# Performance work log

Hardware: AMD Instinct MI355X
Metric: run time of the kernel (lower is better)

The kernel has to match this reference:

```python
import jax, jax.numpy as jnp
import numpy as np

LN_EPS = 1e-5
NEG_INF = -1e38

def _layer_norm(x, g, b):
    mu = x.mean(-1, keepdims=True)
    var = ((x - mu) ** 2).mean(-1, keepdims=True)
    return (x - mu) * jax.lax.rsqrt(var + LN_EPS) * g + b

def _wkv(w, u, k, v):
    # w,u: [C]; k,v: [B,T,C]. Numerically-stable RWKV WKV scan over T.
    B, T, C = k.shape
    kt = jnp.swapaxes(k, 0, 1)  # [T,B,C]
    vt = jnp.swapaxes(v, 0, 1)
    aa0 = jnp.zeros((B, C), k.dtype)
    bb0 = jnp.zeros((B, C), k.dtype)
    pp0 = jnp.full((B, C), NEG_INF, k.dtype)

    def step(carry, inp):
        aa, bb, pp = carry
        kk, vv = inp
        p = jnp.maximum(pp, u + kk)
        e1 = jnp.exp(pp - p)
        e2 = jnp.exp(u + kk - p)
        y = (e1 * aa + e2 * vv) / (e1 + e2)
        p2 = jnp.maximum(pp + w, w + kk)
        e1u = jnp.exp(pp + w - p2)
        e2u = jnp.exp(w + kk - p2)
        aa2 = e1u * aa + e2u * vv
        bb2 = e1u + e2u
        pp2 = p2 + jnp.log(bb2)
        return (aa2, bb2, pp2), y

    _, ys = jax.lax.scan(step, (aa0, bb0, pp0), (kt, vt))
    return jnp.swapaxes(ys, 0, 1)  # [B,T,C]

def _shift(h):
    # x_prev: zero-pad one step at the front (state=None path)
    return jnp.pad(h[:, :-1, :], ((0, 0), (1, 0), (0, 0)))

def setup_inputs() -> dict:
    key = jax.random.key(0)
    B, T, C = 8, 2048, 1024
    ks = jax.random.split(key, 12)
    s = 0.02
    return {
        "x": jax.random.normal(ks[0], (B, T, C), jnp.float32),
        "time_decay": jax.random.normal(ks[1], (C,), jnp.float32) * 0.01,
        "time_first": jax.random.normal(ks[2], (C,), jnp.float32) * 0.01,
        "w_tk": jax.random.normal(ks[3], (C, C), jnp.float32) * s,
        "w_tv": jax.random.normal(ks[4], (C, C), jnp.float32) * s,
        "w_tr": jax.random.normal(ks[5], (C, C), jnp.float32) * s,
        "w_ck": jax.random.normal(ks[6], (C, 4 * C), jnp.float32) * s,
        "w_cv": jax.random.normal(ks[7], (4 * C, C), jnp.float32) * s,
        "w_cr": jax.random.normal(ks[8], (C, C), jnp.float32) * s,
        "ln1_g": jnp.ones((C,), jnp.float32),
        "ln1_b": jnp.zeros((C,), jnp.float32),
        "ln2_g": jnp.ones((C,), jnp.float32),
        "ln2_b": jnp.zeros((C,), jnp.float32),
        "mix_k": jnp.ones((1, 1, C), jnp.float32),
        "mix_v": jnp.ones((1, 1, C), jnp.float32),
        "mix_r": jnp.ones((1, 1, C), jnp.float32),
        "cmix_k": jnp.ones((1, 1, C), jnp.float32),
        "cmix_r": jnp.ones((1, 1, C), jnp.float32),
    }

def reference(x, time_decay, time_first, w_tk, w_tv, w_tr, w_ck, w_cv, w_cr,
              ln1_g, ln1_b, ln2_g, ln2_b, mix_k, mix_v, mix_r, cmix_k, cmix_r):
    # --- time mixing (residual branch 1); dropout is identity at eval ---
    h = _layer_norm(x, ln1_g, ln1_b)
    hp = _shift(h)
    xk = h * mix_k + hp * (1.0 - mix_k)
    xv = h * mix_v + hp * (1.0 - mix_v)
    xr = h * mix_r + hp * (1.0 - mix_r)
    k = xk @ w_tk
    v = xv @ w_tv
    r = jax.nn.sigmoid(xr @ w_tr)
    y = _wkv(time_decay, time_first, k, v)
    x = x + r * y
    # --- channel mixing (residual branch 2) ---
    h2 = _layer_norm(x, ln2_g, ln2_b)
    hp2 = _shift(h2)
    ck = h2 * cmix_k + hp2 * (1.0 - cmix_k)
    cr = h2 * cmix_r + hp2 * (1.0 - cmix_r)
    kk = jnp.square(jax.nn.relu(ck @ w_ck))  # [B,T,4C]
    x = x + jax.nn.sigmoid(cr @ w_cr) * (kk @ w_cv)
    return x
```

## Files before the change

kernel.cpp:

```cpp
#include <hip/hip_runtime.h>
#include <hip/hip_bf16.h>
#include <stdint.h>

#define LN_EPS 1e-5f

typedef __attribute__((ext_vector_type(8))) __bf16 bf16x8;
typedef __attribute__((ext_vector_type(8))) short short8;
typedef __attribute__((ext_vector_type(4))) float floatx4;

__device__ __forceinline__ ushort f2bf(float f) {
    __hip_bfloat16 h = __float2bfloat16(f);
    return *reinterpret_cast<ushort*>(&h);
}
__device__ __forceinline__ float bf2f(ushort u) {
    return __builtin_bit_cast(float, ((unsigned int)u) << 16);
}

__device__ __forceinline__ void gload16(const void* g, void* l) {
#if __has_builtin(__builtin_amdgcn_global_load_lds)
    __builtin_amdgcn_global_load_lds(
        (const __attribute__((address_space(1))) unsigned int*)g,
        (__attribute__((address_space(3))) unsigned int*)l, 16, 0, 0);
#else
    *(int4*)l = *(const int4*)g;
#endif
}

#define SBAR __builtin_amdgcn_s_barrier()
#define SCHED0 __builtin_amdgcn_sched_barrier(0)
#define WAIT_LGKM0 asm volatile("s_waitcnt lgkmcnt(0)" ::: "memory")
#define WAIT_VM4 asm volatile("s_waitcnt vmcnt(4)" ::: "memory")
#define WAIT_VM0 asm volatile("s_waitcnt vmcnt(0)" ::: "memory")

#define STAGE_A(h, t)                                                        \
    do {                                                                     \
        ushort* _d = &lds[((((t) & 1) * 2 + 0) * 2 + (h)) * 8192];           \
        const long _o = (long)(h) * 128 * lda + (long)(t) * 64;              \
        gload16(aS0 + _o, _d + tid * 8);                                     \
        gload16(aS1 + _o, _d + (tid + 512) * 8);                             \
    } while (0)
#define STAGE_B(h, t)                                                        \
    do {                                                                     \
        ushort* _d = &lds[((((t) & 1) * 2 + 1) * 2 + (h)) * 8192];           \
        const long _o = (long)(h) * 128 * ldb + (long)(t) * 64;              \
        gload16(bS0 + _o, _d + tid * 8);                                     \
        gload16(bS1 + _o, _d + (tid + 512) * 8);                             \
    } while (0)
#define GEMM_LDA(MB)                                                         \
    _Pragma("unroll") for (int mi = 0; mi < 4; ++mi)                         \
    _Pragma("unroll") for (int ks = 0; ks < 2; ++ks)                         \
        a[mi][ks] = __builtin_bit_cast(                                      \
            bf16x8, *(const short8*)&ldsA[((MB) + mi) * 1024 + ks * 512 + aoff]);
#define GEMM_LDB(NB)                                                         \
    _Pragma("unroll") for (int ni = 0; ni < 2; ++ni)                         \
    _Pragma("unroll") for (int ks = 0; ks < 2; ++ks)                         \
        b[(NB) + ni][ks] = __builtin_bit_cast(                               \
            bf16x8, *(const short8*)&ldsB[((NB) + ni) * 1024 + ks * 512 + boff]);
#define GEMM_MFMA(MB, NB)                                                    \
    __builtin_amdgcn_s_setprio(1);                                           \
    _Pragma("unroll") for (int mi = 0; mi < 4; ++mi)                         \
    _Pragma("unroll") for (int ni = 0; ni < 2; ++ni)                         \
    _Pragma("unroll") for (int ks = 0; ks < 2; ++ks)                         \
        acc[(MB) + mi][(NB) + ni] = __builtin_amdgcn_mfma_f32_16x16x32_bf16( \
            a[mi][ks], b[(NB) + ni][ks], acc[(MB) + mi][(NB) + ni], 0, 0, 0);\
    __builtin_amdgcn_s_setprio(0);

template <int EPI>
__global__ __launch_bounds__(512, 2) void gemm256(
    const ushort* __restrict__ A, const ushort* __restrict__ Bt,
    int K, int lda, int ldb, int ldc,
    float* __restrict__ outF, ushort* __restrict__ outB,
    const float* __restrict__ add0, const ushort* __restrict__ mul0) {
    extern __shared__ ushort lds[];

    const int tid  = threadIdx.x;
    const int lane = tid & 63;
    const int quad = lane >> 4;
    const int l16  = lane & 15;
    const int wv   = tid >> 6;
    const int wmi  = wv >> 2;
    const int wni  = wv & 3;
    const long m0 = (long)blockIdx.y * 256;
    const long n0 = (long)blockIdx.x * 256;

    floatx4 acc[8][4];
#pragma unroll
    for (int i = 0; i < 8; ++i)
#pragma unroll
        for (int j = 0; j < 4; ++j) acc[i][j] = (floatx4)0.f;

    const int j1 = tid + 512;
    const int r0 = ((tid >> 7) << 4) + (tid & 15);
    const int c0 = (tid >> 4) & 7;
    const int col0 = (c0 & 3) * 8 + (c0 >> 2) * 32;
    const int r1 = ((j1 >> 7) << 4) + (j1 & 15);
    const int c1 = (j1 >> 4) & 7;
    const int col1 = (c1 & 3) * 8 + (c1 >> 2) * 32;
    const ushort* aS0 = A + (m0 + r0) * (long)lda + col0;
    const ushort* aS1 = A + (m0 + r1) * (long)lda + col1;
    const ushort* bS0 = Bt + (n0 + r0) * (long)ldb + col0;
    const ushort* bS1 = Bt + (n0 + r1) * (long)ldb + col1;

    const int aoff = quad * 128 + l16 * 8;
    const int boff = (wni & 1) * 4096 + quad * 128 + l16 * 8;

    const int NT = K >> 6;

    STAGE_A(0, 0); STAGE_A(1, 0);
    STAGE_B(0, 0); STAGE_B(1, 0);
    if (NT > 1) { STAGE_B(0, 1); STAGE_B(1, 1); WAIT_VM4; }
    else        { WAIT_VM0; }
    SBAR;

    bf16x8 a[4][2], b[4][2];
    for (int kt = 0; kt < NT; ++kt) {
        const int d = kt & 1;
        const ushort* ldsA = &lds[((d * 2 + 0) * 2 + wmi) * 8192];
        const ushort* ldsB = &lds[((d * 2 + 1) * 2 + (wni >> 1)) * 8192];

        GEMM_LDA(0)
        GEMM_LDB(0)
        if (kt + 1 < NT) STAGE_A(0, kt + 1);
        SBAR; WAIT_LGKM0; SCHED0;
        GEMM_MFMA(0, 0)
        SCHED0; SBAR;

        GEMM_LDB(2)
        if (kt + 1 < NT) STAGE_A(1, kt + 1);
        SBAR; WAIT_LGKM0; SCHED0;
        GEMM_MFMA(0, 2)
        SCHED0; SBAR;

        GEMM_LDA(4)
        if (kt + 2 < NT) STAGE_B(0, kt + 2);
        SBAR; WAIT_LGKM0; SCHED0;
        GEMM_MFMA(4, 2)
        SCHED0; SBAR;

        if (kt + 2 < NT) STAGE_B(1, kt + 2);
        if (kt < NT - 2) { WAIT_VM4; } else { WAIT_VM0; }
        SBAR; SCHED0;
        GEMM_MFMA(4, 0)
        SCHED0; SBAR;
    }

#pragma unroll
    for (int mi = 0; mi < 8; ++mi) {
#pragma unroll
        for (int ni = 0; ni < 4; ++ni) {
            const long n = n0 + wni * 64 + ni * 16 + l16;
#pragma unroll
            for (int r = 0; r < 4; ++r) {
                const long m = m0 + wmi * 128 + mi * 16 + quad * 4 + r;
                const long idx = m * (long)ldc + n;
                float v = acc[mi][ni][r];
                if constexpr (EPI == 0) {
                    outB[idx] = f2bf(v);
                } else if constexpr (EPI == 1) {
                    outB[idx] = f2bf(1.f / (1.f + __expf(-v)));
                } else if constexpr (EPI == 2) {
                    float t = fmaxf(v, 0.f);
                    outB[idx] = f2bf(t * t);
                } else if constexpr (EPI == 3) {
                    outF[idx] = add0[idx] + bf2f(mul0[idx]) * v;
                }
            }
        }
    }
}

__global__ __launch_bounds__(256) void ln_mix3(
    const float* __restrict__ x, const float* __restrict__ g,
    const float* __restrict__ be,
    const float* __restrict__ mx0, const float* __restrict__ mx1,
    const float* __restrict__ mx2,
    ushort* __restrict__ o0, ushort* __restrict__ o1, ushort* __restrict__ o2,
    int T, int C) {
    const long row = blockIdx.x;
    const int t = (int)(row % T);
    const int tid = threadIdx.x;
    const int i0 = tid * 4;

    floatx4 xc = *(const floatx4*)&x[row * C + i0];
    floatx4 xp = (floatx4)0.f;
    if (t > 0) xp = *(const floatx4*)&x[(row - 1) * C + i0];

    float sc = xc.x + xc.y + xc.z + xc.w;
    float qc = xc.x * xc.x + xc.y * xc.y + xc.z * xc.z + xc.w * xc.w;
    float sp = xp.x + xp.y + xp.z + xp.w;
    float qp = xp.x * xp.x + xp.y * xp.y + xp.z * xp.z + xp.w * xp.w;

#pragma unroll
    for (int off = 32; off; off >>= 1) {
        sc += __shfl_xor(sc, off);
        qc += __shfl_xor(qc, off);
        sp += __shfl_xor(sp, off);
        qp += __shfl_xor(qp, off);
    }
    __shared__ float part[4][4];
    const int wv = tid >> 6;
    if ((tid & 63) == 0) {
        part[wv][0] = sc; part[wv][1] = qc; part[wv][2] = sp; part[wv][3] = qp;
    }
    __syncthreads();
    sc = part[0][0] + part[1][0] + part[2][0] + part[3][0];
    qc = part[0][1] + part[1][1] + part[2][1] + part[3][1];
    sp = part[0][2] + part[1][2] + part[2][2] + part[3][2];
    qp = part[0][3] + part[1][3] + part[2][3] + part[3][3];

    const float invC = 1.f / (float)C;
    float muc = sc * invC;
    float rsc = rsqrtf(qc * invC - muc * muc + LN_EPS);
    float mup = sp * invC;
    float rsp = rsqrtf(qp * invC - mup * mup + LN_EPS);

    floatx4 gv = *(const floatx4*)&g[i0];
    floatx4 bv = *(const floatx4*)&be[i0];
    floatx4 hc = (xc - muc) * rsc * gv + bv;
    floatx4 hp = (floatx4)0.f;
    if (t > 0) hp = (xp - mup) * rsp * gv + bv;

    {
        floatx4 mk = *(const floatx4*)&mx0[i0];
        floatx4 v = hc * mk + hp * (1.f - mk);
        ushort4 pk;
        pk.x = f2bf(v.x); pk.y = f2bf(v.y); pk.z = f2bf(v.z); pk.w = f2bf(v.w);
        *(ushort4*)&o0[row * C + i0] = pk;
    }
    {
        floatx4 mk = *(const floatx4*)&mx1[i0];
        floatx4 v = hc * mk + hp * (1.f - mk);
        ushort4 pk;
        pk.x = f2bf(v.x); pk.y = f2bf(v.y); pk.z = f2bf(v.z); pk.w = f2bf(v.w);
        *(ushort4*)&o1[row * C + i0] = pk;
    }
    {
        floatx4 mk = *(const floatx4*)&mx2[i0];
        floatx4 v = hc * mk + hp * (1.f - mk);
        ushort4 pk;
        pk.x = f2bf(v.x); pk.y = f2bf(v.y); pk.z = f2bf(v.z); pk.w = f2bf(v.w);
        *(ushort4*)&o2[row * C + i0] = pk;
    }
}

__global__ __launch_bounds__(256) void ln_mix_add(
    const float* __restrict__ x, const ushort* __restrict__ ry,
    const float* __restrict__ g, const float* __restrict__ be,
    const float* __restrict__ mx0, const float* __restrict__ mx1,
    float* __restrict__ outx,
    ushort* __restrict__ o0, ushort* __restrict__ o1, int T, int C) {
    const long row = blockIdx.x;
    const int t = (int)(row % T);
    const int tid = threadIdx.x;
    const int i0 = tid * 4;

    floatx4 xc = *(const floatx4*)&x[row * C + i0];
    ushort4 rc = *(const ushort4*)&ry[row * C + i0];
    xc.x += bf2f(rc.x); xc.y += bf2f(rc.y); xc.z += bf2f(rc.z); xc.w += bf2f(rc.w);
    *(floatx4*)&outx[row * C + i0] = xc;

    floatx4 xp = (floatx4)0.f;
    if (t > 0) {
        xp = *(const floatx4*)&x[(row - 1) * C + i0];
        ushort4 rp = *(const ushort4*)&ry[(row - 1) * C + i0];
        xp.x += bf2f(rp.x); xp.y += bf2f(rp.y); xp.z += bf2f(rp.z); xp.w += bf2f(rp.w);
    }

    float sc = xc.x + xc.y + xc.z + xc.w;
    float qc = xc.x * xc.x + xc.y * xc.y + xc.z * xc.z + xc.w * xc.w;
    float sp = xp.x + xp.y + xp.z + xp.w;
    float qp = xp.x * xp.x + xp.y * xp.y + xp.z * xp.z + xp.w * xp.w;

#pragma unroll
    for (int off = 32; off; off >>= 1) {
        sc += __shfl_xor(sc, off);
        qc += __shfl_xor(qc, off);
        sp += __shfl_xor(sp, off);
        qp += __shfl_xor(qp, off);
    }
    __shared__ float part[4][4];
    const int wv = tid >> 6;
    if ((tid & 63) == 0) {
        part[wv][0] = sc; part[wv][1] = qc; part[wv][2] = sp; part[wv][3] = qp;
    }
    __syncthreads();
    sc = part[0][0] + part[1][0] + part[2][0] + part[3][0];
    qc = part[0][1] + part[1][1] + part[2][1] + part[3][1];
    sp = part[0][2] + part[1][2] + part[2][2] + part[3][2];
    qp = part[0][3] + part[1][3] + part[2][3] + part[3][3];

    const float invC = 1.f / (float)C;
    float muc = sc * invC;
    float rsc = rsqrtf(qc * invC - muc * muc + LN_EPS);
    float mup = sp * invC;
    float rsp = rsqrtf(qp * invC - mup * mup + LN_EPS);

    floatx4 gv = *(const floatx4*)&g[i0];
    floatx4 bv = *(const floatx4*)&be[i0];
    floatx4 hc = (xc - muc) * rsc * gv + bv;
    floatx4 hp = (floatx4)0.f;
    if (t > 0) hp = (xp - mup) * rsp * gv + bv;

    {
        floatx4 mk = *(const floatx4*)&mx0[i0];
        floatx4 v = hc * mk + hp * (1.f - mk);
        ushort4 pk;
        pk.x = f2bf(v.x); pk.y = f2bf(v.y); pk.z = f2bf(v.z); pk.w = f2bf(v.w);
        *(ushort4*)&o0[row * C + i0] = pk;
    }
    {
        floatx4 mk = *(const floatx4*)&mx1[i0];
        floatx4 v = hc * mk + hp * (1.f - mk);
        ushort4 pk;
        pk.x = f2bf(v.x); pk.y = f2bf(v.y); pk.z = f2bf(v.z); pk.w = f2bf(v.w);
        *(ushort4*)&o1[row * C + i0] = pk;
    }
}


__global__ __launch_bounds__(256) void wkv_pp_local(
    const float* __restrict__ w, const ushort* __restrict__ k,
    float* __restrict__ pp_loc, int C, int L) {
    const int g = blockIdx.x * 256 + threadIdx.x;
    const int c = g % C;
    const long seg = g / C;
    const float L2E = 1.4426950408889634f;
    const float w2 = w[c] * L2E;
    const ushort* kp = k + seg * L * C + c;
    float pp = -1e38f;
    for (int j = 0; j < L; ++j) {
        float kk = bf2f(kp[(long)j * C]) * L2E;
        float ppw = pp + w2;
        float wk = w2 + kk;
        float p2 = fmaxf(ppw, wk);
        pp = p2 + log2f(exp2f(ppw - p2) + exp2f(wk - p2));
    }
    pp_loc[g] = pp;
}

__global__ __launch_bounds__(256) void wkv_pp_compose(
    const float* __restrict__ w, const float* __restrict__ pp_loc,
    float* __restrict__ pp_in, int C, int SEG, int L) {
    const int g = blockIdx.x * 256 + threadIdx.x;
    const int c = g % C;
    const long b = g / C;
    const float wL = w[c] * 1.4426950408889634f * (float)L;
    float pp = -1e38f;
    for (int s = 0; s < SEG; ++s) {
        const long idx = (b * SEG + s) * C + c;
        pp_in[idx] = pp;
        float lhs = pp + wL;
        float rhs = pp_loc[idx];
        float m = fmaxf(lhs, rhs);
        pp = m + log2f(exp2f(lhs - m) + exp2f(rhs - m));
    }
}

__global__ __launch_bounds__(256) void wkv_ab_local(
    const float* __restrict__ w, const ushort* __restrict__ k,
    const ushort* __restrict__ v, const float* __restrict__ pp_in,
    float* __restrict__ alpha, float* __restrict__ beta, int C, int L) {
    const int g = blockIdx.x * 256 + threadIdx.x;
    const int c = g % C;
    const long seg = g / C;
    const float L2E = 1.4426950408889634f;
    const float w2 = w[c] * L2E;
    const ushort* kp = k + seg * L * C + c;
    const ushort* vp = v + seg * L * C + c;
    float pp = pp_in[g];
    float al = 1.f, be = 0.f;
    for (int j = 0; j < L; ++j) {
        float kk = bf2f(kp[(long)j * C]) * L2E;
        float vv = bf2f(vp[(long)j * C]);
        float ppw = pp + w2;
        float wk = w2 + kk;
        float p2 = fmaxf(ppw, wk);
        float e1u = exp2f(ppw - p2);
        float e2u = exp2f(wk - p2);
        al *= e1u;
        be = e1u * be + e2u * vv;
        pp = p2 + log2f(e1u + e2u);
    }
    alpha[g] = al;
    beta[g] = be;
}

__global__ __launch_bounds__(256) void wkv_aa_compose(
    const float* __restrict__ alpha, const float* __restrict__ beta,
    float* __restrict__ aa_in, int C, int SEG) {
    const int g = blockIdx.x * 256 + threadIdx.x;
    const int c = g % C;
    const long b = g / C;
    float aa = 0.f;
    for (int s = 0; s < SEG; ++s) {
        const long idx = (b * SEG + s) * C + c;
        aa_in[idx] = aa;
        aa = alpha[idx] * aa + beta[idx];
    }
    (void)c;
}

__global__ __launch_bounds__(256) void wkv_emit(
    const float* __restrict__ w, const float* __restrict__ u,
    const ushort* __restrict__ k, const ushort* __restrict__ v,
    const ushort* __restrict__ r, const float* __restrict__ aa_in,
    const float* __restrict__ pp_in, ushort* __restrict__ ry, int C, int L) {
    const int g = blockIdx.x * 256 + threadIdx.x;
    const int c = g % C;
    const long seg = g / C;
    const float L2E = 1.4426950408889634f;
    const float w2 = w[c] * L2E;
    const float u2 = u[c] * L2E;
    const long base = seg * L * C + c;
    const ushort* kp = k + base;
    const ushort* vp = v + base;
    const ushort* rp = r + base;
    ushort* op = ry + base;
    float aa = aa_in[g];
    float pp = pp_in[g];
    for (int j = 0; j < L; ++j) {
        const long o = (long)j * C;
        float kk = bf2f(kp[o]) * L2E;
        float vv = bf2f(vp[o]);
        float uk = u2 + kk;
        float p = fmaxf(pp, uk);
        float e1 = exp2f(pp - p);
        float e2 = exp2f(uk - p);
        float y = __fdividef(e1 * aa + e2 * vv, e1 + e2);
        op[o] = f2bf(bf2f(rp[o]) * y);
        float ppw = pp + w2;
        float wk = w2 + kk;
        float p2 = fmaxf(ppw, wk);
        float e1u = exp2f(ppw - p2);
        float e2u = exp2f(wk - p2);
        aa = e1u * aa + e2u * vv;
        pp = p2 + log2f(e1u + e2u);
    }
}

__global__ __launch_bounds__(256) void transpose_bf16(
    const float* __restrict__ in, ushort* __restrict__ out, int K, int N) {
    __shared__ float tile[32][33];
    const int tx = threadIdx.x, ty = threadIdx.y;
    const long k0 = (long)blockIdx.y * 32, n0 = (long)blockIdx.x * 32;
#pragma unroll
    for (int i = 0; i < 4; i++)
        tile[ty + i * 8][tx] = in[(k0 + ty + i * 8) * N + n0 + tx];
    __syncthreads();
#pragma unroll
    for (int i = 0; i < 4; i++)
        out[(n0 + ty + i * 8) * K + k0 + tx] = f2bf(tile[tx][ty + i * 8]);
}

extern "C" void kernel_launch(void* const* d_in, const int* in_sizes, int n_in,
                              void* d_out, int out_size, void* d_ws, size_t ws_size,
                              hipStream_t stream) {
    const float* x      = (const float*)d_in[0];
    const float* tdecay = (const float*)d_in[1];
    const float* tfirst = (const float*)d_in[2];
    const float* w_tk   = (const float*)d_in[3];
    const float* w_tv   = (const float*)d_in[4];
    const float* w_tr   = (const float*)d_in[5];
    const float* w_ck   = (const float*)d_in[6];
    const float* w_cv   = (const float*)d_in[7];
    const float* w_cr   = (const float*)d_in[8];
    const float* ln1g   = (const float*)d_in[9];
    const float* ln1b   = (const float*)d_in[10];
    const float* ln2g   = (const float*)d_in[11];
    const float* ln2b   = (const float*)d_in[12];
    const float* mixk   = (const float*)d_in[13];
    const float* mixv   = (const float*)d_in[14];
    const float* mixr   = (const float*)d_in[15];
    const float* cmixk  = (const float*)d_in[16];
    const float* cmixr  = (const float*)d_in[17];
    float* out = (float*)d_out;

    const int C  = in_sizes[1];
    const long M = (long)in_sizes[0] / C;
    const int T  = 2048;
    const int B  = (int)(M / T);
    const int H  = 2 * C;
    const int SEG = 64;
    const int L  = T / SEG;
    const int NSEG = B * SEG;

    static bool s_attr = []() {
        (void)hipFuncSetAttribute((const void*)gemm256<0>,
                                  hipFuncAttributeMaxDynamicSharedMemorySize, 131072);
        (void)hipFuncSetAttribute((const void*)gemm256<1>,
                                  hipFuncAttributeMaxDynamicSharedMemorySize, 131072);
        (void)hipFuncSetAttribute((const void*)gemm256<2>,
                                  hipFuncAttributeMaxDynamicSharedMemorySize, 131072);
        (void)hipFuncSetAttribute((const void*)gemm256<3>,
                                  hipFuncAttributeMaxDynamicSharedMemorySize, 131072);
        return true;
    }();
    (void)s_attr;
    const int SMEM = 131072;

    const size_t MBy = 1024ull * 1024ull;
    char* w8 = (char*)d_ws;
    ushort* wT_tk  = (ushort*)(w8 + 0 * MBy);
    ushort* wT_tv  = (ushort*)(w8 + 2 * MBy);
    ushort* wT_tr  = (ushort*)(w8 + 4 * MBy);
    ushort* wT_cr  = (ushort*)(w8 + 6 * MBy);
    ushort* wT_ck  = (ushort*)(w8 + 8 * MBy);
    ushort* wT_cv0 = (ushort*)(w8 + 16 * MBy);
    ushort* wT_cv1 = (ushort*)(w8 + 20 * MBy);
    ushort* xk     = (ushort*)(w8 + 24 * MBy);
    ushort* xv     = (ushort*)(w8 + 56 * MBy);
    ushort* xr     = (ushort*)(w8 + 88 * MBy);
    ushort* kbuf   = (ushort*)(w8 + 120 * MBy);
    ushort* vbuf   = (ushort*)(w8 + 152 * MBy);
    ushort* rbuf   = (ushort*)(w8 + 24 * MBy);
    float*  pp_loc = (float*)(w8 + 56 * MBy);
    float*  pp_in  = (float*)(w8 + 58 * MBy);
    float*  alpha  = (float*)(w8 + 60 * MBy);
    float*  beta   = (float*)(w8 + 62 * MBy);
    float*  aa_in  = (float*)(w8 + 64 * MBy);
    ushort* ry     = (ushort*)(w8 + 88 * MBy);
    ushort* ck     = (ushort*)(w8 + 120 * MBy);
    ushort* cr     = (ushort*)(w8 + 152 * MBy);
    ushort* scr    = (ushort*)(w8 + 24 * MBy);
    ushort* kkbuf  = (ushort*)(w8 + 56 * MBy);

    dim3 tb(32, 8);
    transpose_bf16<<<dim3(C / 32, C / 32), tb, 0, stream>>>(w_tk, wT_tk, C, C);
    transpose_bf16<<<dim3(C / 32, C / 32), tb, 0, stream>>>(w_tv, wT_tv, C, C);
    transpose_bf16<<<dim3(C / 32, C / 32), tb, 0, stream>>>(w_tr, wT_tr, C, C);
    transpose_bf16<<<dim3(C / 32, C / 32), tb, 0, stream>>>(w_cr, wT_cr, C, C);
    transpose_bf16<<<dim3(4 * C / 32, C / 32), tb, 0, stream>>>(w_ck, wT_ck, C, 4 * C);
    transpose_bf16<<<dim3(C / 32, H / 32), tb, 0, stream>>>(w_cv, wT_cv0, H, C);
    transpose_bf16<<<dim3(C / 32, H / 32), tb, 0, stream>>>(w_cv + (long)H * C, wT_cv1, H, C);

    ln_mix3<<<(int)M, 256, 0, stream>>>(x, ln1g, ln1b, mixk, mixv, mixr,
                                        xk, xv, xr, T, C);

    dim3 g256(C / 256, (int)(M / 256));
    gemm256<0><<<g256, 512, SMEM, stream>>>(xk, wT_tk, C, C, C, C,
                                            nullptr, kbuf, nullptr, nullptr);
    gemm256<0><<<g256, 512, SMEM, stream>>>(xv, wT_tv, C, C, C, C,
                                            nullptr, vbuf, nullptr, nullptr);
    gemm256<1><<<g256, 512, SMEM, stream>>>(xr, wT_tr, C, C, C, C,
                                            nullptr, rbuf, nullptr, nullptr);

    const int segthreads = NSEG * C;
    wkv_pp_local<<<segthreads / 256, 256, 0, stream>>>(tdecay, kbuf, pp_loc, C, L);
    wkv_pp_compose<<<(B * C) / 256, 256, 0, stream>>>(tdecay, pp_loc, pp_in, C, SEG, L);
    wkv_ab_local<<<segthreads / 256, 256, 0, stream>>>(tdecay, kbuf, vbuf, pp_in,
                                                       alpha, beta, C, L);
    wkv_aa_compose<<<(B * C) / 256, 256, 0, stream>>>(alpha, beta, aa_in, C, SEG);
    wkv_emit<<<segthreads / 256, 256, 0, stream>>>(tdecay, tfirst, kbuf, vbuf, rbuf,
                                                   aa_in, pp_in, ry, C, L);

    ln_mix_add<<<(int)M, 256, 0, stream>>>(x, ry, ln2g, ln2b, cmixk, cmixr,
                                           out, ck, cr, T, C);

    gemm256<1><<<g256, 512, SMEM, stream>>>(cr, wT_cr, C, C, C, C,
                                            nullptr, scr, nullptr, nullptr);

    for (int h = 0; h < 2; ++h) {
        const ushort* wck_h = wT_ck + (long)h * H * C;
        const ushort* wcv_h = (h == 0) ? wT_cv0 : wT_cv1;
        gemm256<2><<<dim3(H / 256, (int)(M / 256)), 512, SMEM, stream>>>(
            ck, wck_h, C, C, C, H, nullptr, kkbuf, nullptr, nullptr);
        gemm256<3><<<g256, 512, SMEM, stream>>>(
            kkbuf, wcv_h, H, H, H, C, out, nullptr, out, scr);
    }
}
```

Baseline: 902.0 us.

## Replace 256x256 GEMM with 128x128 triple-buffered tile and XCD-aware block remap

Swaps the 512-thread 256x256-tile GEMM (dynamic 128KB LDS, double-buffered K=64 slices with interleaved partial MFMA phases) for a 256-thread 128x128 tile. The new kernel uses K=32 slices in a three-slot static LDS ring and a block-index swizzle that spreads consecutive tiles across the eight XCDs. It aims for higher occupancy, more blocks per GEMM, and simpler overlap of loads with compute. In exchange, each tile reuses operands less, so global and L2 traffic goes up, and the loop takes two barriers for every small K step.

Result: slower. 1.154 ms (+28.0%).

```diff
diff --git a/kernel.cpp b/kernel.cpp
--- a/kernel.cpp
+++ b/kernel.cpp
@@ -28,130 +28,113 @@
 
 #define SBAR __builtin_amdgcn_s_barrier()
 #define SCHED0 __builtin_amdgcn_sched_barrier(0)
-#define WAIT_LGKM0 asm volatile("s_waitcnt lgkmcnt(0)" ::: "memory")
+#define WAIT_VM8 asm volatile("s_waitcnt vmcnt(8)" ::: "memory")
 #define WAIT_VM4 asm volatile("s_waitcnt vmcnt(4)" ::: "memory")
 #define WAIT_VM0 asm volatile("s_waitcnt vmcnt(0)" ::: "memory")
 
-#define STAGE_A(h, t)                                                        \
-    do {                                                                     \
-        ushort* _d = &lds[((((t) & 1) * 2 + 0) * 2 + (h)) * 8192];           \
-        const long _o = (long)(h) * 128 * lda + (long)(t) * 64;              \
-        gload16(aS0 + _o, _d + tid * 8);                                     \
-        gload16(aS1 + _o, _d + (tid + 512) * 8);                             \
-    } while (0)
-#define STAGE_B(h, t)                                                        \
-    do {                                                                     \
-        ushort* _d = &lds[((((t) & 1) * 2 + 1) * 2 + (h)) * 8192];           \
-        const long _o = (long)(h) * 128 * ldb + (long)(t) * 64;              \
-        gload16(bS0 + _o, _d + tid * 8);                                     \
-        gload16(bS1 + _o, _d + (tid + 512) * 8);                             \
-    } while (0)
-#define GEMM_LDA(MB)                                                         \
-    _Pragma("unroll") for (int mi = 0; mi < 4; ++mi)                         \
-    _Pragma("unroll") for (int ks = 0; ks < 2; ++ks)                         \
-        a[mi][ks] = __builtin_bit_cast(                                      \
-            bf16x8, *(const short8*)&ldsA[((MB) + mi) * 1024 + ks * 512 + aoff]);
-#define GEMM_LDB(NB)                                                         \
-    _Pragma("unroll") for (int ni = 0; ni < 2; ++ni)                         \
-    _Pragma("unroll") for (int ks = 0; ks < 2; ++ks)                         \
-        b[(NB) + ni][ks] = __builtin_bit_cast(                               \
-            bf16x8, *(const short8*)&ldsB[((NB) + ni) * 1024 + ks * 512 + boff]);
-#define GEMM_MFMA(MB, NB)                                                    \
-    __builtin_amdgcn_s_setprio(1);                                           \
-    _Pragma("unroll") for (int mi = 0; mi < 4; ++mi)                         \
-    _Pragma("unroll") for (int ni = 0; ni < 2; ++ni)                         \
-    _Pragma("unroll") for (int ks = 0; ks < 2; ++ks)                         \
-        acc[(MB) + mi][(NB) + ni] = __builtin_amdgcn_mfma_f32_16x16x32_bf16( \
-            a[mi][ks], b[(NB) + ni][ks], acc[(MB) + mi][(NB) + ni], 0, 0, 0);\
-    __builtin_amdgcn_s_setprio(0);
-
 template <int EPI>
-__global__ __launch_bounds__(512, 2) void gemm256(
+__global__ __launch_bounds__(256, 3) void gemm128(
     const ushort* __restrict__ A, const ushort* __restrict__ Bt,
     int K, int lda, int ldb, int ldc,
     float* __restrict__ outF, ushort* __restrict__ outB,
     const float* __restrict__ add0, const ushort* __restrict__ mul0) {
-    extern __shared__ ushort lds[];
+    __shared__ __align__(16) ushort lds[3 * 8192];
 
     const int tid  = threadIdx.x;
     const int lane = tid & 63;
     const int quad = lane >> 4;
     const int l16  = lane & 15;
     const int wv   = tid >> 6;
-    const int wmi  = wv >> 2;
-    const int wni  = wv & 3;
-    const long m0 = (long)blockIdx.y * 256;
-    const long n0 = (long)blockIdx.x * 256;
-
-    floatx4 acc[8][4];
-#pragma unroll
-    for (int i = 0; i < 8; ++i)
+    const int wmi  = wv >> 1;
+    const int wni  = wv & 1;
+
+    const int gx  = gridDim.x;
+    const int nwg = gx * gridDim.y;
+    int bid = blockIdx.y * gx + blockIdx.x;
+    bid = (bid & 7) * (nwg >> 3) + (bid >> 3);
+    const long m0 = (long)(bid / gx) * 128;
+    const long n0 = (long)(bid % gx) * 128;
+
+    floatx4 acc[4][4];
+#pragma unroll
+    for (int i = 0; i < 4; ++i)
 #pragma unroll
         for (int j = 0; j < 4; ++j) acc[i][j] = (floatx4)0.f;
 
-    const int j1 = tid + 512;
-    const int r0 = ((tid >> 7) << 4) + (tid & 15);
-    const int c0 = (tid >> 4) & 7;
-    const int col0 = (c0 & 3) * 8 + (c0 >> 2) * 32;
-    const int r1 = ((j1 >> 7) << 4) + (j1 & 15);
-    const int c1 = (j1 >> 4) & 7;
-    const int col1 = (c1 & 3) * 8 + (c1 >> 2) * 32;
-    const ushort* aS0 = A + (m0 + r0) * (long)lda + col0;
-    const ushort* aS1 = A + (m0 + r1) * (long)lda + col1;
-    const ushort* bS0 = Bt + (n0 + r0) * (long)ldb + col0;
-    const ushort* bS1 = Bt + (n0 + r1) * (long)ldb + col1;
+    const int rs = ((tid >> 6) << 4) + (tid & 15);
+    const int cs = ((tid >> 4) & 3) * 8;
+    const ushort* aP0 = A + (m0 + rs) * (long)lda + cs;
+    const ushort* aP1 = aP0 + 64 * (long)lda;
+    const ushort* bP0 = Bt + (n0 + rs) * (long)ldb + cs;
+    const ushort* bP1 = bP0 + 64 * (long)ldb;
+    const int dA0 = tid * 8, dA1 = tid * 8 + 2048;
+    const int dB0 = 4096 + tid * 8, dB1 = 4096 + tid * 8 + 2048;
 
     const int aoff = quad * 128 + l16 * 8;
-    const int boff = (wni & 1) * 4096 + quad * 128 + l16 * 8;
-
-    const int NT = K >> 6;
-
-    STAGE_A(0, 0); STAGE_A(1, 0);
-    STAGE_B(0, 0); STAGE_B(1, 0);
-    if (NT > 1) { STAGE_B(0, 1); STAGE_B(1, 1); WAIT_VM4; }
-    else        { WAIT_VM0; }
-    SBAR;
-
-    bf16x8 a[4][2], b[4][2];
-    for (int kt = 0; kt < NT; ++kt) {
-        const int d = kt & 1;
-        const ushort* ldsA = &lds[((d * 2 + 0) * 2 + wmi) * 8192];
-        const ushort* ldsB = &lds[((d * 2 + 1) * 2 + (wni >> 1)) * 8192];
-
-        GEMM_LDA(0)
-        GEMM_LDB(0)
-        if (kt + 1 < NT) STAGE_A(0, kt + 1);
-        SBAR; WAIT_LGKM0; SCHED0;
-        GEMM_MFMA(0, 0)
-        SCHED0; SBAR;
-
-        GEMM_LDB(2)
-        if (kt + 1 < NT) STAGE_A(1, kt + 1);
-        SBAR; WAIT_LGKM0; SCHED0;
-        GEMM_MFMA(0, 2)
-        SCHED0; SBAR;
-
-        GEMM_LDA(4)
-        if (kt + 2 < NT) STAGE_B(0, kt + 2);
-        SBAR; WAIT_LGKM0; SCHED0;
-        GEMM_MFMA(4, 2)
-        SCHED0; SBAR;
-
-        if (kt + 2 < NT) STAGE_B(1, kt + 2);
-        if (kt < NT - 2) { WAIT_VM4; } else { WAIT_VM0; }
-        SBAR; SCHED0;
-        GEMM_MFMA(4, 0)
-        SCHED0; SBAR;
-    }
-
-#pragma unroll
-    for (int mi = 0; mi < 8; ++mi) {
+    const int NT = K >> 5;
+
+#define STAGE128(t, sl)                                                       \
+    do {                                                                      \
+        const long _ko = (long)(t) * 32;                                      \
+        ushort* _d = &lds[(sl) * 8192];                                       \
+        gload16(aP0 + _ko, _d + dA0);                                         \
+        gload16(aP1 + _ko, _d + dA1);                                         \
+        gload16(bP0 + _ko, _d + dB0);                                         \
+        gload16(bP1 + _ko, _d + dB1);                                         \
+    } while (0)
+
+    STAGE128(0, 0);
+    STAGE128(1, 1);
+
+    int sl = 0;
+    int st = 2;
+    for (int t = 0; t < NT; ++t) {
+        SBAR;
+        SCHED0;
+        if (t + 2 < NT) {
+            STAGE128(t + 2, st);
+            WAIT_VM8;
+        } else if (t + 1 < NT) {
+            WAIT_VM4;
+        } else {
+            WAIT_VM0;
+        }
+        SBAR;
+        SCHED0;
+
+        const ushort* buf = &lds[sl * 8192];
+        bf16x8 a[4], b[4];
+#pragma unroll
+        for (int mi = 0; mi < 4; ++mi)
+            a[mi] = __builtin_bit_cast(
+                bf16x8, *(const short8*)&buf[(wmi * 4 + mi) * 512 + aoff]);
+#pragma unroll
+        for (int ni = 0; ni < 4; ++ni)
+            b[ni] = __builtin_bit_cast(
+                bf16x8, *(const short8*)&buf[4096 + (wni * 4 + ni) * 512 + aoff]);
+
+        __builtin_amdgcn_s_setprio(1);
+#pragma unroll
+        for (int mi = 0; mi < 4; ++mi)
+#pragma unroll
+            for (int ni = 0; ni < 4; ++ni)
+                acc[mi][ni] = __builtin_amdgcn_mfma_f32_16x16x32_bf16(
+                    a[mi], b[ni], acc[mi][ni], 0, 0, 0);
+        __builtin_amdgcn_s_setprio(0);
+        SCHED0;
+
+        sl = (sl == 2) ? 0 : sl + 1;
+        st = (st == 2) ? 0 : st + 1;
+    }
+
+#pragma unroll
+    for (int mi = 0; mi < 4; ++mi) {
 #pragma unroll
         for (int ni = 0; ni < 4; ++ni) {
             const long n = n0 + wni * 64 + ni * 16 + l16;
 #pragma unroll
             for (int r = 0; r < 4; ++r) {
-                const long m = m0 + wmi * 128 + mi * 16 + quad * 4 + r;
+                const long m = m0 + wmi * 64 + mi * 16 + quad * 4 + r;
                 const long idx = m * (long)ldc + n;
                 float v = acc[mi][ni][r];
                 if constexpr (EPI == 0) {
@@ -167,6 +150,7 @@
             }
         }
     }
+#undef STAGE128
 }
 
 __global__ __launch_bounds__(256) void ln_mix3(
@@ -484,20 +468,6 @@
     const int L  = T / SEG;
     const int NSEG = B * SEG;
 
-    static bool s_attr = []() {
-        (void)hipFuncSetAttribute((const void*)gemm256<0>,
-                                  hipFuncAttributeMaxDynamicSharedMemorySize, 131072);
-        (void)hipFuncSetAttribute((const void*)gemm256<1>,
-                                  hipFuncAttributeMaxDynamicSharedMemorySize, 131072);
-        (void)hipFuncSetAttribute((const void*)gemm256<2>,
-                                  hipFuncAttributeMaxDynamicSharedMemorySize, 131072);
-        (void)hipFuncSetAttribute((const void*)gemm256<3>,
-                                  hipFuncAttributeMaxDynamicSharedMemorySize, 131072);
-        return true;
-    }();
-    (void)s_attr;
-    const int SMEM = 131072;
-
     const size_t MBy = 1024ull * 1024ull;
     char* w8 = (char*)d_ws;
     ushort* wT_tk  = (ushort*)(w8 + 0 * MBy);
@@ -536,13 +506,13 @@
     ln_mix3<<<(int)M, 256, 0, stream>>>(x, ln1g, ln1b, mixk, mixv, mixr,
                                         xk, xv, xr, T, C);
 
-    dim3 g256(C / 256, (int)(M / 256));
-    gemm256<0><<<g256, 512, SMEM, stream>>>(xk, wT_tk, C, C, C, C,
-                                            nullptr, kbuf, nullptr, nullptr);
-    gemm256<0><<<g256, 512, SMEM, stream>>>(xv, wT_tv, C, C, C, C,
-                                            nullptr, vbuf, nullptr, nullptr);
-    gemm256<1><<<g256, 512, SMEM, stream>>>(xr, wT_tr, C, C, C, C,
-                                            nullptr, rbuf, nullptr, nullptr);
+    dim3 g128(C / 128, (int)(M / 128));
+    gemm128<0><<<g128, 256, 0, stream>>>(xk, wT_tk, C, C, C, C,
+                                         nullptr, kbuf, nullptr, nullptr);
+    gemm128<0><<<g128, 256, 0, stream>>>(xv, wT_tv, C, C, C, C,
+                                         nullptr, vbuf, nullptr, nullptr);
+    gemm128<1><<<g128, 256, 0, stream>>>(xr, wT_tr, C, C, C, C,
+                                         nullptr, rbuf, nullptr, nullptr);
 
     const int segthreads = NSEG * C;
     wkv_pp_local<<<segthreads / 256, 256, 0, stream>>>(tdecay, kbuf, pp_loc, C, L);
@@ -556,15 +526,15 @@
     ln_mix_add<<<(int)M, 256, 0, stream>>>(x, ry, ln2g, ln2b, cmixk, cmixr,
                                            out, ck, cr, T, C);
 
-    gemm256<1><<<g256, 512, SMEM, stream>>>(cr, wT_cr, C, C, C, C,
-                                            nullptr, scr, nullptr, nullptr);
+    gemm128<1><<<g128, 256, 0, stream>>>(cr, wT_cr, C, C, C, C,
+                                         nullptr, scr, nullptr, nullptr);
 
     for (int h = 0; h < 2; ++h) {
         const ushort* wck_h = wT_ck + (long)h * H * C;
         const ushort* wcv_h = (h == 0) ? wT_cv0 : wT_cv1;
-        gemm256<2><<<dim3(H / 256, (int)(M / 256)), 512, SMEM, stream>>>(
+        gemm128<2><<<dim3(H / 128, (int)(M / 128)), 256, 0, stream>>>(
             ck, wck_h, C, C, C, H, nullptr, kkbuf, nullptr, nullptr);
-        gemm256<3><<<g256, 512, SMEM, stream>>>(
+        gemm128<3><<<g128, 256, 0, stream>>>(
             kkbuf, wcv_h, H, H, H, C, out, nullptr, out, scr);
     }
 }
```
